# Performance work log

Measured on AMD Instinct MI355X. Metric: run time of the kernel, lower is better.

## Reference

```python
import jax, jax.numpy as jnp
import numpy as np

EMBED_DIM = 2048
N_HEAD = 16
N_KV_HEAD = 4
HEAD_DIM = EMBED_DIM // N_HEAD  # 128
GROUP = N_HEAD // N_KV_HEAD     # 4
SCALE = HEAD_DIM ** -0.5
B, T = 2, 2048


def setup_inputs() -> dict:
    key = jax.random.key(0)
    ks = jax.random.split(key, 5)
    s = 0.02
    # weights stored as [in, out] (y = x @ W); equivalent to torch Linear W.T
    return {
        "x": jax.random.normal(ks[0], (B, T, EMBED_DIM), jnp.float32),
        "Wq": jax.random.normal(ks[1], (EMBED_DIM, EMBED_DIM), jnp.float32) * s,
        "Wk": jax.random.normal(ks[2], (EMBED_DIM, N_KV_HEAD * HEAD_DIM), jnp.float32) * s,
        "Wv": jax.random.normal(ks[3], (EMBED_DIM, N_KV_HEAD * HEAD_DIM), jnp.float32) * s,
        "Wo": jax.random.normal(ks[4], (EMBED_DIM, EMBED_DIM), jnp.float32) * s,
    }


def reference(x, Wq, Wk, Wv, Wo):
    # Prefill path (T>1, no cache): GQA causal attention, eval mode (dropout=0).
    Bq, Tq, C = x.shape
    q = (x @ Wq).reshape(Bq, Tq, N_HEAD, HEAD_DIM).transpose(0, 2, 1, 3)      # (B,Hq,T,D)
    k = (x @ Wk).reshape(Bq, Tq, N_KV_HEAD, HEAD_DIM).transpose(0, 2, 1, 3)  # (B,Hkv,T,D)
    v = (x @ Wv).reshape(Bq, Tq, N_KV_HEAD, HEAD_DIM).transpose(0, 2, 1, 3)
    # expand_kv: each kv head repeated GROUP times consecutively
    k = jnp.repeat(k, GROUP, axis=1)  # (B,Hq,T,D)
    v = jnp.repeat(v, GROUP, axis=1)
    scores = jnp.einsum("bhqd,bhkd->bhqk", q, k) * SCALE
    causal = jnp.tril(jnp.ones((Tq, Tq), dtype=bool))
    scores = jnp.where(causal[None, None], scores, jnp.finfo(scores.dtype).min)
    probs = jax.nn.softmax(scores, axis=-1)
    atten = jnp.einsum("bhqk,bhkd->bhqd", probs, v)
    atten = atten.transpose(0, 2, 1, 3).reshape(Bq, Tq, C)
    out = atten @ Wo
    return out
```

## Files before the change

### kernel.cpp

```cpp
#include <hip/hip_runtime.h>

typedef unsigned short u16;
typedef unsigned int   u32;
typedef __attribute__((ext_vector_type(4))) float  f32x4;
typedef __attribute__((ext_vector_type(8))) __bf16 bf16x8;

#define EMBED 2048
#define NH    16
#define NKV   4
#define HD    128
#define TT    2048
#define BB    2
#define MROWS (BB*TT)
#define QSCALE 0.08838834764831845f

static __device__ __forceinline__ u16 f2b(float f){
  union { float f; u32 u; } v; v.f = f;
  u32 u = v.u;
  u32 r = u + 0x7FFFu + ((u >> 16) & 1u);
  return (u16)(r >> 16);
}

__global__ __launch_bounds__(256) void cvt_f32_bf16(const float* __restrict__ in,
                                                    u16* __restrict__ out, int n4){
  int i = blockIdx.x * 256 + threadIdx.x;
  if (i >= n4) return;
  float4 v = ((const float4*)in)[i];
  uint2 o;
  o.x = (u32)f2b(v.x) | ((u32)f2b(v.y) << 16);
  o.y = (u32)f2b(v.z) | ((u32)f2b(v.w) << 16);
  ((uint2*)out)[i] = o;
}

__global__ __launch_bounds__(256) void trans_w(const float* __restrict__ in,
                                               u16* __restrict__ out, int R, int C){
  __shared__ u16 tile[32][33];
  int c0 = blockIdx.x * 32, r0 = blockIdx.y * 32;
  int tx = threadIdx.x & 31, ty = threadIdx.x >> 5;
  #pragma unroll
  for (int j = 0; j < 32; j += 8)
    tile[ty + j][tx] = f2b(in[(size_t)(r0 + ty + j) * C + c0 + tx]);
  __syncthreads();
  #pragma unroll
  for (int j = 0; j < 32; j += 8)
    out[(size_t)(c0 + ty + j) * R + r0 + tx] = tile[tx][ty + j];
}

__global__ __launch_bounds__(256) void trans_v(const u16* __restrict__ in,
                                               u16* __restrict__ out){
  __shared__ u16 tile[32][33];
  int d0 = (blockIdx.x & 3) * 32;
  int t0 = ((blockIdx.x >> 2) & 63) * 32;
  int bh = blockIdx.x >> 8;
  const u16* ip = in  + (size_t)bh * TT * HD;
  u16*       op = out + (size_t)bh * TT * HD;
  int tx = threadIdx.x & 31, ty = threadIdx.x >> 5;
  #pragma unroll
  for (int j = 0; j < 32; j += 8)
    tile[ty + j][tx] = ip[(size_t)(t0 + ty + j) * HD + d0 + tx];
  __syncthreads();
  #pragma unroll
  for (int j = 0; j < 32; j += 8)
    op[(size_t)(d0 + ty + j) * TT + t0 + tx] = tile[tx][ty + j];
}

template<int EPI>
__global__ __launch_bounds__(256)
void gemm_bt(const u16* __restrict__ A, const u16* __restrict__ Bt,
             void* __restrict__ outp, int N, int K, int Hh, float scale){
  __shared__ __align__(16) u16 As[2][128*32];
  __shared__ __align__(16) u16 Bs[2][128*32];
  int tid  = threadIdx.x;
  int lane = tid & 63, w = tid >> 6;
  int nwg = gridDim.x;
  int bid = blockIdx.x;
  bid = (bid & 7) * (nwg >> 3) + (bid >> 3);
  int nbn  = N >> 7;
  int brow = (bid / nbn) * 128;
  int bcol = (bid % nbn) * 128;

  auto stage = [&](int buf, int kt){
    #pragma unroll
    for (int j = 0; j < 2; ++j){
      int boff  = w * 2048 + j * 1024;
      int chunk = (boff >> 4) + lane;
      int row   = chunk >> 2;
      int cko   = chunk & 3;
      const u16* ga = A  + (size_t)(brow + row) * K + kt + cko * 8;
      const u16* gb = Bt + (size_t)(bcol + row) * K + kt + cko * 8;
      __builtin_amdgcn_global_load_lds((__attribute__((address_space(1))) void*)(void*)ga,
          (__attribute__((address_space(3))) void*)(void*)(&As[buf][boff >> 1]), 16, 0, 0);
      __builtin_amdgcn_global_load_lds((__attribute__((address_space(1))) void*)(void*)gb,
          (__attribute__((address_space(3))) void*)(void*)(&Bs[buf][boff >> 1]), 16, 0, 0);
    }
  };

  int lr = lane & 15, lg = lane >> 4, lk = lg * 8;
  int wr = (w >> 1) * 64, wc = (w & 1) * 64;

  f32x4 acc[4][4];
  #pragma unroll
  for (int m = 0; m < 4; ++m)
    #pragma unroll
    for (int n = 0; n < 4; ++n)
      #pragma unroll
      for (int r = 0; r < 4; ++r) acc[m][n][r] = 0.f;

  int NT = K >> 5;
  stage(0, 0);
  asm volatile("s_waitcnt vmcnt(0)" ::: "memory");
  __syncthreads();
  int cur = 0;
  for (int t = 0; t < NT; ++t){
    if (t + 1 < NT) stage(cur ^ 1, (t + 1) * 32);
    const u16* as = As[cur];
    const u16* bs = Bs[cur];
    bf16x8 af[4], bfv[4];
    #pragma unroll
    for (int m = 0; m < 4; ++m) af[m]  = *(const bf16x8*)(as + (wr + m*16 + lr)*32 + lk);
    #pragma unroll
    for (int n = 0; n < 4; ++n) bfv[n] = *(const bf16x8*)(bs + (wc + n*16 + lr)*32 + lk);
    #pragma unroll
    for (int m = 0; m < 4; ++m)
      #pragma unroll
      for (int n = 0; n < 4; ++n)
        acc[m][n] = __builtin_amdgcn_mfma_f32_16x16x32_bf16(af[m], bfv[n], acc[m][n], 0, 0, 0);
    asm volatile("s_waitcnt vmcnt(0)" ::: "memory");
    __syncthreads();
    cur ^= 1;
  }

  if (EPI == 0){
    float* o = (float*)outp;
    #pragma unroll
    for (int m = 0; m < 4; ++m)
      #pragma unroll
      for (int r = 0; r < 4; ++r){
        int rowg = brow + wr + m*16 + lg*4 + r;
        float* orow = o + (size_t)rowg * N + bcol + wc + lr;
        #pragma unroll
        for (int n = 0; n < 4; ++n) orow[n*16] = acc[m][n][r];
      }
  } else {
    u16* o = (u16*)outp;
    #pragma unroll
    for (int m = 0; m < 4; ++m)
      #pragma unroll
      for (int r = 0; r < 4; ++r){
        int rowg = brow + wr + m*16 + lg*4 + r;
        int b = rowg >> 11;
        int t = rowg & (TT - 1);
        #pragma unroll
        for (int n = 0; n < 4; ++n){
          int colg = bcol + wc + n*16 + lr;
          int h = colg >> 7, d = colg & 127;
          o[(((size_t)b * Hh + h) * TT + t) * HD + d] = f2b(acc[m][n][r] * scale);
        }
      }
  }
}

__global__ __launch_bounds__(256)
void attn_kernel(const u16* __restrict__ qb, const u16* __restrict__ kb,
                 const u16* __restrict__ vtb, u16* __restrict__ ob){
  __shared__ __align__(16) u16 Ks[2][64*128];
  __shared__ __align__(16) u16 Vs[2][128*64];
  __shared__ __align__(16) u16 pl[4][16*88];
  int tid = threadIdx.x, lane = tid & 63, w = tid >> 6;
  int nwg = gridDim.x;
  int bid = blockIdx.x;
  bid = (bid & 7) * (nwg >> 3) + (bid >> 3);
  int pair = bid & 15;
  int h    = (bid >> 4) & 15;
  int b    = bid >> 8;
  int hkv  = h >> 2;
  int lr = lane & 15, lg = lane >> 4, lk = lg * 8;
  int sw = (lr & 7) << 3;

  const u16* qbase = qb  + ((size_t)b * NH  + h  ) * TT * HD;
  const u16* kbase = kb  + ((size_t)b * NKV + hkv) * TT * HD;
  const u16* vbase = vtb + ((size_t)b * NKV + hkv) * HD * TT;

  auto stage = [&](int buf, int kt){
    #pragma unroll
    for (int i = 0; i < 4; ++i){
      int c  = i * 256 + tid;
      int ub = (i * 256 + w * 64) * 8;
      int kr = c >> 4, kc = (c & 15) ^ (kr & 7);
      const u16* gk = kbase + (size_t)(kt * 64 + kr) * HD + kc * 8;
      __builtin_amdgcn_global_load_lds((__attribute__((address_space(1))) void*)(void*)gk,
          (__attribute__((address_space(3))) void*)(void*)(&Ks[buf][ub]), 16, 0, 0);
      int vr = c >> 3, vc = (c & 7) ^ (vr & 7);
      const u16* gv = vbase + (size_t)vr * TT + kt * 64 + vc * 8;
      __builtin_amdgcn_global_load_lds((__attribute__((address_space(1))) void*)(void*)gv,
          (__attribute__((address_space(3))) void*)(void*)(&Vs[buf][ub]), 16, 0, 0);
    }
  };

  __bf16* plw = (__bf16*)pl[w];

  for (int half = 0; half < 2; ++half){
    int qt = half ? (31 - pair) : pair;
    int q0 = qt * 64 + w * 16;

    bf16x8 aq[4];
    #pragma unroll
    for (int s = 0; s < 4; ++s)
      aq[s] = *(const bf16x8*)(qbase + (size_t)(q0 + lr) * HD + s*32 + lk);

    f32x4 o_acc[8];
    #pragma unroll
    for (int dt = 0; dt < 8; ++dt)
      #pragma unroll
      for (int r = 0; r < 4; ++r) o_acc[dt][r] = 0.f;
    float mrow[4], lrow[4];
    #pragma unroll
    for (int r = 0; r < 4; ++r){ mrow[r] = -1e30f; lrow[r] = 0.f; }

    stage(0, 0);
    asm volatile("s_waitcnt vmcnt(0)" ::: "memory");
    __syncthreads();
    int cur = 0;
    for (int kt = 0; kt <= qt; ++kt){
      if (kt < qt) stage(cur ^ 1, kt + 1);
      const u16* ks = Ks[cur];
      f32x4 sc[4];
      #pragma unroll
      for (int c = 0; c < 4; ++c)
        #pragma unroll
        for (int r = 0; r < 4; ++r) sc[c][r] = 0.f;
      #pragma unroll
      for (int c = 0; c < 4; ++c){
        const u16* kp = ks + (c*16 + lr) * 128;
        #pragma unroll
        for (int s = 0; s < 4; ++s){
          bf16x8 kf = *(const bf16x8*)(kp + (((s*32) + lk) ^ sw));
          sc[c] = __builtin_amdgcn_mfma_f32_16x16x32_bf16(aq[s], kf, sc[c], 0, 0, 0);
        }
      }
      if (kt == qt){
        #pragma unroll
        for (int c = 0; c < 4; ++c){
          int kvg = kt*64 + c*16 + lr;
          #pragma unroll
          for (int r = 0; r < 4; ++r){
            int qg = q0 + lg*4 + r;
            if (kvg > qg) sc[c][r] = -1e30f;
          }
        }
      }
      #pragma unroll
      for (int r = 0; r < 4; ++r){
        float tm = fmaxf(fmaxf(sc[0][r], sc[1][r]), fmaxf(sc[2][r], sc[3][r]));
        tm = fmaxf(tm, __shfl_xor(tm, 1));
        tm = fmaxf(tm, __shfl_xor(tm, 2));
        tm = fmaxf(tm, __shfl_xor(tm, 4));
        tm = fmaxf(tm, __shfl_xor(tm, 8));
        float mnew  = fmaxf(mrow[r], tm);
        float alpha = __expf(mrow[r] - mnew);
        mrow[r] = mnew;
        float rs = 0.f;
        #pragma unroll
        for (int c = 0; c < 4; ++c){
          float p = __expf(sc[c][r] - mnew);
          rs += p;
          plw[(lg*4 + r)*88 + c*16 + lr] = (__bf16)p;
        }
        rs += __shfl_xor(rs, 1); rs += __shfl_xor(rs, 2);
        rs += __shfl_xor(rs, 4); rs += __shfl_xor(rs, 8);
        lrow[r] = lrow[r] * alpha + rs;
        #pragma unroll
        for (int dt = 0; dt < 8; ++dt) o_acc[dt][r] *= alpha;
      }
      asm volatile("s_waitcnt lgkmcnt(0)" ::: "memory");
      bf16x8 pa[2];
      #pragma unroll
      for (int kk = 0; kk < 2; ++kk)
        pa[kk] = *(const bf16x8*)((const u16*)plw + lr*88 + kk*32 + lk);
      const u16* vs = Vs[cur];
      #pragma unroll
      for (int dt = 0; dt < 8; ++dt){
        const u16* vp = vs + (dt*16 + lr) * 64;
        #pragma unroll
        for (int kk = 0; kk < 2; ++kk){
          bf16x8 vf = *(const bf16x8*)(vp + (((kk*32) + lk) ^ sw));
          o_acc[dt] = __builtin_amdgcn_mfma_f32_16x16x32_bf16(pa[kk], vf, o_acc[dt], 0, 0, 0);
        }
      }
      asm volatile("s_waitcnt vmcnt(0)" ::: "memory");
      __syncthreads();
      cur ^= 1;
    }
    #pragma unroll
    for (int r = 0; r < 4; ++r){
      float inv = 1.0f / lrow[r];
      int t = q0 + lg*4 + r;
      size_t base = ((size_t)b * TT + t) * EMBED + h * HD;
      #pragma unroll
      for (int dt = 0; dt < 8; ++dt)
        ob[base + dt*16 + lr] = f2b(o_acc[dt][r] * inv);
    }
  }
}

extern "C" void kernel_launch(void* const* d_in, const int* in_sizes, int n_in,
                              void* d_out, int out_size, void* d_ws, size_t ws_size,
                              hipStream_t stream){
  const float* x  = (const float*)d_in[0];
  const float* Wq = (const float*)d_in[1];
  const float* Wk = (const float*)d_in[2];
  const float* Wv = (const float*)d_in[3];
  const float* Wo = (const float*)d_in[4];

  char* ws = (char*)d_ws;
  size_t off = 0;
  auto alloc = [&](size_t bytes){ void* p = ws + off; off += (bytes + 255) & ~(size_t)255; return p; };
  u16* xb  = (u16*)alloc((size_t)MROWS * EMBED * 2);
  u16* Wqt = (u16*)alloc((size_t)EMBED * EMBED * 2);
  u16* Wkt = (u16*)alloc((size_t)512 * EMBED * 2);
  u16* Wvt = (u16*)alloc((size_t)512 * EMBED * 2);
  u16* Wot = (u16*)alloc((size_t)EMBED * EMBED * 2);
  u16* qb  = (u16*)alloc((size_t)BB * NH  * TT * HD * 2);
  u16* kb  = (u16*)alloc((size_t)BB * NKV * TT * HD * 2);
  u16* vb  = (u16*)alloc((size_t)BB * NKV * TT * HD * 2);
  u16* vtb = (u16*)alloc((size_t)BB * NKV * TT * HD * 2);
  u16* ob  = (u16*)alloc((size_t)MROWS * EMBED * 2);

  cvt_f32_bf16<<<(MROWS*EMBED/4 + 255)/256, 256, 0, stream>>>(x, xb, MROWS*EMBED/4);
  trans_w<<<dim3(EMBED/32, EMBED/32), 256, 0, stream>>>(Wq, Wqt, EMBED, EMBED);
  trans_w<<<dim3(512/32,   EMBED/32), 256, 0, stream>>>(Wk, Wkt, EMBED, 512);
  trans_w<<<dim3(512/32,   EMBED/32), 256, 0, stream>>>(Wv, Wvt, EMBED, 512);
  trans_w<<<dim3(EMBED/32, EMBED/32), 256, 0, stream>>>(Wo, Wot, EMBED, EMBED);

  gemm_bt<1><<<(MROWS/128)*(EMBED/128), 256, 0, stream>>>(xb, Wqt, qb, EMBED, EMBED, NH,  QSCALE);
  gemm_bt<1><<<(MROWS/128)*(512/128),   256, 0, stream>>>(xb, Wkt, kb, 512,   EMBED, NKV, 1.0f);
  gemm_bt<1><<<(MROWS/128)*(512/128),   256, 0, stream>>>(xb, Wvt, vb, 512,   EMBED, NKV, 1.0f);
  trans_v<<<4*64*BB*NKV, 256, 0, stream>>>(vb, vtb);

  attn_kernel<<<BB*NH*16, 256, 0, stream>>>(qb, kb, vtb, ob);

  gemm_bt<0><<<(MROWS/128)*(EMBED/128), 256, 0, stream>>>(ob, Wot, d_out, EMBED, EMBED, 0, 1.0f);
}
```

Before: 387.0 us.

## Fuse QKV projection GEMM, batch weight transposes, add lazy softmax rescale and setprio

Concatenates the transposed Wq, Wk and Wv into one [3072, EMBED] weight so a single GEMM launch computes Q, K and V. Its epilogue picks the destination head buffer and scale per 128-column block. Weight transposes are merged into two launches using a z grid dimension. The attention kernel now skips the online-softmax rescale of the output accumulator unless some row max grows by more than 8, and raises wave priority around its MFMA blocks. The lazy rescale lets exp values reach up to e^8 before rescaling, which relies on fp32 and bf16 range being enough.

```diff
diff --git a/kernel.cpp b/kernel.cpp
--- a/kernel.cpp
+++ b/kernel.cpp
@@ -13,6 +13,9 @@
 #define BB    2
 #define MROWS (BB*TT)
 #define QSCALE 0.08838834764831845f
+
+#define QELEMS ((size_t)BB*NH*TT*HD)
+#define KELEMS ((size_t)BB*NKV*TT*HD)
 
 static __device__ __forceinline__ u16 f2b(float f){
   union { float f; u32 u; } v; v.f = f;
@@ -32,8 +35,11 @@
   ((uint2*)out)[i] = o;
 }
 
-__global__ __launch_bounds__(256) void trans_w(const float* __restrict__ in,
-                                               u16* __restrict__ out, int R, int C){
+__global__ __launch_bounds__(256) void trans_w2(const float* __restrict__ in0, u16* __restrict__ out0,
+                                                const float* __restrict__ in1, u16* __restrict__ out1,
+                                                int R, int C){
+  const float* in = blockIdx.z ? in1 : in0;
+  u16*        out = blockIdx.z ? out1 : out0;
   __shared__ u16 tile[32][33];
   int c0 = blockIdx.x * 32, r0 = blockIdx.y * 32;
   int tx = threadIdx.x & 31, ty = threadIdx.x >> 5;
@@ -67,7 +73,7 @@
 template<int EPI>
 __global__ __launch_bounds__(256)
 void gemm_bt(const u16* __restrict__ A, const u16* __restrict__ Bt,
-             void* __restrict__ outp, int N, int K, int Hh, float scale){
+             void* __restrict__ outp, int N, int K){
   __shared__ __align__(16) u16 As[2][128*32];
   __shared__ __align__(16) u16 Bs[2][128*32];
   int tid  = threadIdx.x;
@@ -142,19 +148,24 @@
         for (int n = 0; n < 4; ++n) orow[n*16] = acc[m][n][r];
       }
   } else {
-    u16* o = (u16*)outp;
+    u16* qb = (u16*)outp;
+    u16* kb = qb + QELEMS;
+    u16* vb = kb + KELEMS;
+    int hb = bcol >> 7;
+    int b  = brow >> 11;
+    u16* hp; float s;
+    if (hb < 16)      { hp = qb + ((size_t)(b*NH  +  hb     )) * TT * HD; s = QSCALE; }
+    else if (hb < 20) { hp = kb + ((size_t)(b*NKV + (hb-16))) * TT * HD; s = 1.0f; }
+    else              { hp = vb + ((size_t)(b*NKV + (hb-20))) * TT * HD; s = 1.0f; }
     #pragma unroll
     for (int m = 0; m < 4; ++m)
       #pragma unroll
       for (int r = 0; r < 4; ++r){
-        int rowg = brow + wr + m*16 + lg*4 + r;
-        int b = rowg >> 11;
-        int t = rowg & (TT - 1);
+        int t = (brow + wr + m*16 + lg*4 + r) & (TT - 1);
         #pragma unroll
         for (int n = 0; n < 4; ++n){
-          int colg = bcol + wc + n*16 + lr;
-          int h = colg >> 7, d = colg & 127;
-          o[(((size_t)b * Hh + h) * TT + t) * HD + d] = f2b(acc[m][n][r] * scale);
+          int d = wc + n*16 + lr;
+          hp[(size_t)t * HD + d] = f2b(acc[m][n][r] * s);
         }
       }
   }
@@ -229,6 +240,7 @@
       for (int c = 0; c < 4; ++c)
         #pragma unroll
         for (int r = 0; r < 4; ++r) sc[c][r] = 0.f;
+      __builtin_amdgcn_s_setprio(1);
       #pragma unroll
       for (int c = 0; c < 4; ++c){
         const u16* kp = ks + (c*16 + lr) * 128;
@@ -238,6 +250,7 @@
           sc[c] = __builtin_amdgcn_mfma_f32_16x16x32_bf16(aq[s], kf, sc[c], 0, 0, 0);
         }
       }
+      __builtin_amdgcn_s_setprio(0);
       if (kt == qt){
         #pragma unroll
         for (int c = 0; c < 4; ++c){
@@ -249,6 +262,7 @@
           }
         }
       }
+      float tmv[4];
       #pragma unroll
       for (int r = 0; r < 4; ++r){
         float tm = fmaxf(fmaxf(sc[0][r], sc[1][r]), fmaxf(sc[2][r], sc[3][r]));
@@ -256,21 +270,33 @@
         tm = fmaxf(tm, __shfl_xor(tm, 2));
         tm = fmaxf(tm, __shfl_xor(tm, 4));
         tm = fmaxf(tm, __shfl_xor(tm, 8));
-        float mnew  = fmaxf(mrow[r], tm);
-        float alpha = __expf(mrow[r] - mnew);
-        mrow[r] = mnew;
+        tmv[r] = tm;
+      }
+      bool need = (tmv[0] > mrow[0] + 8.f) || (tmv[1] > mrow[1] + 8.f) ||
+                  (tmv[2] > mrow[2] + 8.f) || (tmv[3] > mrow[3] + 8.f);
+      if (__any(need ? 1 : 0)){
+        #pragma unroll
+        for (int r = 0; r < 4; ++r){
+          float mnew  = fmaxf(mrow[r], tmv[r]);
+          float alpha = __expf(mrow[r] - mnew);
+          mrow[r] = mnew;
+          lrow[r] *= alpha;
+          #pragma unroll
+          for (int dt = 0; dt < 8; ++dt) o_acc[dt][r] *= alpha;
+        }
+      }
+      #pragma unroll
+      for (int r = 0; r < 4; ++r){
         float rs = 0.f;
         #pragma unroll
         for (int c = 0; c < 4; ++c){
-          float p = __expf(sc[c][r] - mnew);
+          float p = __expf(sc[c][r] - mrow[r]);
           rs += p;
           plw[(lg*4 + r)*88 + c*16 + lr] = (__bf16)p;
         }
         rs += __shfl_xor(rs, 1); rs += __shfl_xor(rs, 2);
         rs += __shfl_xor(rs, 4); rs += __shfl_xor(rs, 8);
-        lrow[r] = lrow[r] * alpha + rs;
-        #pragma unroll
-        for (int dt = 0; dt < 8; ++dt) o_acc[dt][r] *= alpha;
+        lrow[r] += rs;
       }
       asm volatile("s_waitcnt lgkmcnt(0)" ::: "memory");
       bf16x8 pa[2];
@@ -278,6 +304,7 @@
       for (int kk = 0; kk < 2; ++kk)
         pa[kk] = *(const bf16x8*)((const u16*)plw + lr*88 + kk*32 + lk);
       const u16* vs = Vs[cur];
+      __builtin_amdgcn_s_setprio(1);
       #pragma unroll
       for (int dt = 0; dt < 8; ++dt){
         const u16* vp = vs + (dt*16 + lr) * 64;
@@ -287,6 +314,7 @@
           o_acc[dt] = __builtin_amdgcn_mfma_f32_16x16x32_bf16(pa[kk], vf, o_acc[dt], 0, 0, 0);
         }
       }
+      __builtin_amdgcn_s_setprio(0);
       asm volatile("s_waitcnt vmcnt(0)" ::: "memory");
       __syncthreads();
       cur ^= 1;
@@ -315,29 +343,26 @@
   char* ws = (char*)d_ws;
   size_t off = 0;
   auto alloc = [&](size_t bytes){ void* p = ws + off; off += (bytes + 255) & ~(size_t)255; return p; };
-  u16* xb  = (u16*)alloc((size_t)MROWS * EMBED * 2);
-  u16* Wqt = (u16*)alloc((size_t)EMBED * EMBED * 2);
-  u16* Wkt = (u16*)alloc((size_t)512 * EMBED * 2);
-  u16* Wvt = (u16*)alloc((size_t)512 * EMBED * 2);
-  u16* Wot = (u16*)alloc((size_t)EMBED * EMBED * 2);
-  u16* qb  = (u16*)alloc((size_t)BB * NH  * TT * HD * 2);
-  u16* kb  = (u16*)alloc((size_t)BB * NKV * TT * HD * 2);
-  u16* vb  = (u16*)alloc((size_t)BB * NKV * TT * HD * 2);
-  u16* vtb = (u16*)alloc((size_t)BB * NKV * TT * HD * 2);
-  u16* ob  = (u16*)alloc((size_t)MROWS * EMBED * 2);
+  u16* xb    = (u16*)alloc((size_t)MROWS * EMBED * 2);
+  u16* Wqkvt = (u16*)alloc((size_t)3072 * EMBED * 2);
+  u16* Wot   = (u16*)alloc((size_t)EMBED * EMBED * 2);
+  u16* qkv   = (u16*)alloc((QELEMS + 2*KELEMS) * 2);
+  u16* vtb   = (u16*)alloc(KELEMS * 2);
+  u16* ob    = (u16*)alloc((size_t)MROWS * EMBED * 2);
+
+  u16* qb = qkv;
+  u16* kb = qb + QELEMS;
+  u16* vb = kb + KELEMS;
 
   cvt_f32_bf16<<<(MROWS*EMBED/4 + 255)/256, 256, 0, stream>>>(x, xb, MROWS*EMBED/4);
-  trans_w<<<dim3(EMBED/32, EMBED/32), 256, 0, stream>>>(Wq, Wqt, EMBED, EMBED);
-  trans_w<<<dim3(512/32,   EMBED/32), 256, 0, stream>>>(Wk, Wkt, EMBED, 512);
-  trans_w<<<dim3(512/32,   EMBED/32), 256, 0, stream>>>(Wv, Wvt, EMBED, 512);
-  trans_w<<<dim3(EMBED/32, EMBED/32), 256, 0, stream>>>(Wo, Wot, EMBED, EMBED);
-
-  gemm_bt<1><<<(MROWS/128)*(EMBED/128), 256, 0, stream>>>(xb, Wqt, qb, EMBED, EMBED, NH,  QSCALE);
-  gemm_bt<1><<<(MROWS/128)*(512/128),   256, 0, stream>>>(xb, Wkt, kb, 512,   EMBED, NKV, 1.0f);
-  gemm_bt<1><<<(MROWS/128)*(512/128),   256, 0, stream>>>(xb, Wvt, vb, 512,   EMBED, NKV, 1.0f);
+  trans_w2<<<dim3(EMBED/32, EMBED/32, 2), 256, 0, stream>>>(Wq, Wqkvt, Wo, Wot, EMBED, EMBED);
+  trans_w2<<<dim3(512/32,   EMBED/32, 2), 256, 0, stream>>>(Wk, Wqkvt + (size_t)2048*EMBED,
+                                                            Wv, Wqkvt + (size_t)2560*EMBED, EMBED, 512);
+
+  gemm_bt<2><<<(MROWS/128)*(3072/128), 256, 0, stream>>>(xb, Wqkvt, qkv, 3072, EMBED);
   trans_v<<<4*64*BB*NKV, 256, 0, stream>>>(vb, vtb);
 
   attn_kernel<<<BB*NH*16, 256, 0, stream>>>(qb, kb, vtb, ob);
 
-  gemm_bt<0><<<(MROWS/128)*(EMBED/128), 256, 0, stream>>>(ob, Wot, d_out, EMBED, EMBED, 0, 1.0f);
-}
+  gemm_bt<0><<<(MROWS/128)*(EMBED/128), 256, 0, stream>>>(ob, Wot, d_out, EMBED, EMBED);
+}
```

New measurement: 312.8 us. 19.2% less time.
